# Kernel tuning notes

Measured on AMD Instinct MI355X. Metric: run time of the kernel, lower is better.

The kernel has to match this reference:

```python
import jax, jax.numpy as jnp
import numpy as np

DIM_V = 512
NUM_HEADS = 8
LN_EPS = 1e-5


def _layernorm(x):
    # LayerNorm over last dim, no affine (simplified_layer_norm=True)
    mu = jnp.mean(x, axis=-1, keepdims=True)
    var = jnp.mean(jnp.square(x - mu), axis=-1, keepdims=True)
    return (x - mu) * jax.lax.rsqrt(var + LN_EPS)


def setup_inputs() -> dict:
    key = jax.random.key(0)
    ks = jax.random.split(key, 12)
    B, Nq, Nk, dQ, dK, dV = 16, 1024, 1024, 512, 512, DIM_V
    s = 0.02
    return {
        "Q": jax.random.normal(ks[0], (B, Nq, dQ), jnp.float32),
        "K": jax.random.normal(ks[1], (B, Nk, dK), jnp.float32),
        "Wq": jax.random.normal(ks[2], (dQ, dV), jnp.float32) * s,
        "bq": jnp.zeros((dV,), jnp.float32),
        "Wk": jax.random.normal(ks[3], (dK, dV), jnp.float32) * s,
        "bk": jnp.zeros((dV,), jnp.float32),
        "Wv": jax.random.normal(ks[4], (dK, dV), jnp.float32) * s,
        "bv": jnp.zeros((dV,), jnp.float32),
        "Wo": jax.random.normal(ks[5], (dV, dV), jnp.float32) * s,
        "bo": jnp.zeros((dV,), jnp.float32),
    }


def reference(Q, K, Wq, bq, Wk, bk, Wv, bv, Wo, bo):
    H = NUM_HEADS
    dh = DIM_V // H
    q = Q @ Wq + bq            # [B, Nq, dV]
    k = K @ Wk + bk            # [B, Nk, dV]
    v = K @ Wv + bv            # [B, Nk, dV]
    B, Nq, _ = q.shape
    Nk = k.shape[1]
    qh = q.reshape(B, Nq, H, dh)
    kh = k.reshape(B, Nk, H, dh)
    vh = v.reshape(B, Nk, H, dh)
    # NOTE: faithful to source — scale by sqrt(dim_V), not sqrt(head_dim)
    scores = jnp.einsum('bqhd,bkhd->bhqk', qh, kh) / jnp.sqrt(jnp.asarray(DIM_V, q.dtype))
    A = jax.nn.softmax(scores, axis=-1)                    # [B, H, Nq, Nk]
    attn = jnp.einsum('bhqk,bkhd->bqhd', A, vh).reshape(B, Nq, DIM_V)
    O = q + attn               # residual with projected Q
    O = _layernorm(O)          # ln0 (no affine)
    O = O + jax.nn.gelu(O @ Wo + bo, approximate=False)
    O = _layernorm(O)          # ln1 (no affine)
    return O
```

## Files before the change

### kernel.cpp

```cpp
#include <hip/hip_runtime.h>
#include <hip/hip_bf16.h>
#include <math.h>

typedef __bf16 bf16;
typedef __bf16 bf16x8 __attribute__((ext_vector_type(8)));
typedef float  f32x4  __attribute__((ext_vector_type(4)));

#define MFMA16(a,b,c) __builtin_amdgcn_mfma_f32_16x16x32_bf16((a),(b),(c),0,0,0)
#define ATT_SCALE 0.0441941738241592f

__device__ __forceinline__ void async16p(const void* g, void* l) {
    __builtin_amdgcn_global_load_lds((const __attribute__((address_space(1))) void*)g,
                                     (__attribute__((address_space(3))) void*)l,
                                     16, 0, 0);
}

__global__ __launch_bounds__(256) void prep_w_kernel(
    const float* __restrict__ Wq, const float* __restrict__ Wk,
    const float* __restrict__ Wv, const float* __restrict__ Wo,
    bf16* __restrict__ WqT, bf16* __restrict__ WkT,
    bf16* __restrict__ WvT, bf16* __restrict__ WoT)
{
    __shared__ float tile[32][33];
    const int bx = blockIdx.x;
    const float* W; bf16* T;
    switch (bx >> 8) {
      case 0: W=Wq; T=WqT; break;
      case 1: W=Wk; T=WkT; break;
      case 2: W=Wv; T=WvT; break;
      default: W=Wo; T=WoT; break;
    }
    const int rest = bx & 255;
    const int k0 = (rest & 15) * 32, n0 = (rest >> 4) * 32;
    const int tx = threadIdx.x & 31, ty = threadIdx.x >> 5;
    #pragma unroll
    for (int i=0;i<32;i+=8)
        tile[ty+i][tx] = W[(size_t)(k0+ty+i)*512 + n0+tx];
    __syncthreads();
    #pragma unroll
    for (int i=0;i<32;i+=8)
        T[(size_t)(n0+ty+i)*512 + k0+tx] = (bf16)tile[tx][ty+i];
}

__global__ __launch_bounds__(256, 2) void gemm_qkv_kernel(
    const float* __restrict__ Qf, const float* __restrict__ Kf,
    const bf16* __restrict__ WqT, const bf16* __restrict__ WkT,
    const bf16* __restrict__ WvT,
    const float* __restrict__ bq, const float* __restrict__ bk,
    const float* __restrict__ bv,
    bf16* __restrict__ qbb, bf16* __restrict__ kbb, bf16* __restrict__ vT)
{
    __shared__ float As32[128*32];
    __shared__ bf16  Bs0[128*32];
    __shared__ bf16  Bs1[128*32];
    __shared__ bf16  Lt[64][136];
    const bool kv = (blockIdx.z != 0);
    const float* A   = kv ? Kf : Qf;
    const bf16*  BT0 = kv ? WkT : WqT;
    const float* b0  = kv ? bk : bq;
    bf16* C0 = kv ? kbb : qbb;

    const int m0 = blockIdx.x * 128, n0 = blockIdx.y * 128;
    const int tid = threadIdx.x;
    const int lane = tid & 63, wave = tid >> 6;
    const int qd = lane >> 4, lr = lane & 15;
    const int wm = (wave & 1) * 64, wn = (wave >> 1) * 64;

    const float* gA = A + (size_t)(m0 + (tid>>3))*512 + (((tid&7)^((tid>>3)&7))*4);
    float* lA = As32 + wave*256;
    const int bgr = ((tid&3)^((tid>>2)&3))*8;
    const bf16* gB0 = BT0 + (size_t)(n0 + (tid>>2))*512 + bgr;
    const bf16* gB1 = WvT + (size_t)(n0 + (tid>>2))*512 + bgr;
    bf16* lB0 = Bs0 + wave*512;
    bf16* lB1 = Bs1 + wave*512;

    f32x4 acc0[4][4], acc1[4][4];
    #pragma unroll
    for (int i=0;i<4;i++)
      #pragma unroll
      for (int j=0;j<4;j++) { acc0[i][j] = (f32x4){0,0,0,0}; acc1[i][j] = (f32x4){0,0,0,0}; }

    for (int k0 = 0; k0 < 512; k0 += 32) {
        __syncthreads();
        #pragma unroll
        for (int i=0;i<4;i++)
            async16p(gA + k0 + (size_t)i*32*512, lA + i*1024);
        async16p(gB0 + k0,            lB0);
        async16p(gB0 + k0 + 64*512,   lB0 + 2048);
        if (kv) {
            async16p(gB1 + k0,          lB1);
            async16p(gB1 + k0 + 64*512, lB1 + 2048);
        }
        __syncthreads();
        bf16x8 af[4], bf0[4], bf1[4];
        #pragma unroll
        for (int mi=0;mi<4;mi++) {
            int row = wm + mi*16 + lr;
            f32x4 f0 = *(f32x4*)(As32 + row*32 + (((qd*2  )^(lr&7))*4));
            f32x4 f1 = *(f32x4*)(As32 + row*32 + (((qd*2+1)^(lr&7))*4));
            bf16x8 a;
            a[0]=(bf16)f0[0]; a[1]=(bf16)f0[1]; a[2]=(bf16)f0[2]; a[3]=(bf16)f0[3];
            a[4]=(bf16)f1[0]; a[5]=(bf16)f1[1]; a[6]=(bf16)f1[2]; a[7]=(bf16)f1[3];
            af[mi] = a;
        }
        #pragma unroll
        for (int ni=0;ni<4;ni++) {
            int row = wn + ni*16 + lr;
            bf0[ni] = *(bf16x8*)(Bs0 + row*32 + ((qd^(lr&3))*8));
            if (kv) bf1[ni] = *(bf16x8*)(Bs1 + row*32 + ((qd^(lr&3))*8));
        }
        #pragma unroll
        for (int mi=0;mi<4;mi++)
          #pragma unroll
          for (int ni=0;ni<4;ni++) {
            acc0[mi][ni] = MFMA16(af[mi], bf0[ni], acc0[mi][ni]);
            if (kv) acc1[mi][ni] = MFMA16(af[mi], bf1[ni], acc1[mi][ni]);
          }
    }

    #pragma unroll
    for (int ni=0;ni<4;ni++) {
        int n = n0 + wn + ni*16 + lr;
        float bv0 = b0[n];
        #pragma unroll
        for (int mi=0;mi<4;mi++) {
            int mb = m0 + wm + mi*16 + qd*4;
            #pragma unroll
            for (int r=0;r<4;r++)
                C0[(size_t)(mb+r)*512 + n] = (bf16)(acc0[mi][ni][r] + bv0);
        }
    }
    if (kv) {
        const int b = m0 >> 10, tok0 = m0 & 1023;
        const int row = tid >> 2, ch = tid & 3;
        #pragma unroll
        for (int half = 0; half < 2; ++half) {
            __syncthreads();
            if ((wn >> 6) == half) {
                #pragma unroll
                for (int ni=0;ni<4;ni++) {
                    int nl = ni*16 + lr;
                    float bvv = bv[n0 + half*64 + nl];
                    #pragma unroll
                    for (int mi=0;mi<4;mi++)
                      #pragma unroll
                      for (int r=0;r<4;r++)
                        Lt[nl][wm + mi*16 + qd*4 + r] = (bf16)(acc1[mi][ni][r] + bvv);
                }
            }
            __syncthreads();
            const int h = (n0 >> 6) + half;
            bf16* dst = vT + ((size_t)((b*8 + h)*64 + row))*1024 + tok0 + ch*32;
            uint4 x0 = *(uint4*)(&Lt[row][ch*32]);
            uint4 x1 = *(uint4*)(&Lt[row][ch*32 + 8]);
            uint4 x2 = *(uint4*)(&Lt[row][ch*32 + 16]);
            uint4 x3 = *(uint4*)(&Lt[row][ch*32 + 24]);
            *(uint4*)(dst)      = x0;
            *(uint4*)(dst + 8)  = x1;
            *(uint4*)(dst + 16) = x2;
            *(uint4*)(dst + 24) = x3;
        }
    }
}

__global__ __launch_bounds__(256, 4) void attn_kernel(
    const bf16* __restrict__ qb, const bf16* __restrict__ kb,
    const bf16* __restrict__ vT, bf16* __restrict__ attnb)
{
    const int qt = blockIdx.x, h = blockIdx.y, b = blockIdx.z;
    const int tid = threadIdx.x, lane = tid & 63, wave = tid >> 6;
    const int qd = lane >> 4, lr = lane & 15;
    const int q0 = qt*64 + wave*16;

    __shared__ bf16 Ks[64*64];
    __shared__ bf16 Vs[64*64];
    __shared__ bf16 Pl[4][16][72];

    bf16x8 aq0, aq1;
    {
        const bf16* qrow = qb + ((size_t)(b*1024 + q0 + lr))*512 + h*64;
        aq0 = *(const bf16x8*)(qrow + qd*8);
        aq1 = *(const bf16x8*)(qrow + 32 + qd*8);
    }

    const int srow = (tid >> 3) & 7;
    const int sgr  = ((tid&7) ^ srow) * 8;
    const bf16* kgp = kb + ((size_t)(b*1024 + wave*8 + srow))*512 + h*64 + sgr;
    const bf16* vgp = vT + ((size_t)((b*8 + h)*64 + wave*8 + srow))*1024 + sgr;
    bf16* lK = Ks + wave*512;
    bf16* lV = Vs + wave*512;

    f32x4 acc[4];
    #pragma unroll
    for (int i=0;i<4;i++) acc[i] = (f32x4){0,0,0,0};
    float l[4] = {0.f,0.f,0.f,0.f};

    for (int t=0; t<16; ++t) {
        const int kk0 = t*64;
        __syncthreads();
        async16p(kgp + (size_t)kk0*512,            lK);
        async16p(kgp + (size_t)(kk0+32)*512,       lK + 2048);
        async16p(vgp + kk0,                        lV);
        async16p(vgp + (size_t)32*1024 + kk0,      lV + 2048);
        __syncthreads();

        f32x4 s[4];
        #pragma unroll
        for (int ni=0;ni<4;ni++) s[ni] = (f32x4){0,0,0,0};
        #pragma unroll
        for (int ni=0;ni<4;ni++) {
            int row = ni*16 + lr;
            bf16x8 b0 = *(bf16x8*)(Ks + row*64 + (((qd  )^(lr&7))*8));
            bf16x8 b1 = *(bf16x8*)(Ks + row*64 + (((qd+4)^(lr&7))*8));
            s[ni] = MFMA16(aq0, b0, s[ni]);
            s[ni] = MFMA16(aq1, b1, s[ni]);
        }
        #pragma unroll
        for (int ni=0;ni<4;ni++)
          #pragma unroll
          for (int r=0;r<4;r++) {
            float pv = __expf(s[ni][r] * ATT_SCALE);
            s[ni][r] = pv;
            l[r] += pv;
          }
        #pragma unroll
        for (int ni=0;ni<4;ni++)
          #pragma unroll
          for (int r=0;r<4;r++)
            Pl[wave][qd*4+r][ni*16+lr] = (bf16)s[ni][r];
        bf16x8 ap0 = *(bf16x8*)(&Pl[wave][lr][qd*8]);
        bf16x8 ap1 = *(bf16x8*)(&Pl[wave][lr][32+qd*8]);
        #pragma unroll
        for (int ni=0;ni<4;ni++) {
            int row = ni*16 + lr;
            bf16x8 v0 = *(bf16x8*)(Vs + row*64 + (((qd  )^(lr&7))*8));
            bf16x8 v1 = *(bf16x8*)(Vs + row*64 + (((qd+4)^(lr&7))*8));
            acc[ni] = MFMA16(ap0, v0, acc[ni]);
            acc[ni] = MFMA16(ap1, v1, acc[ni]);
        }
    }

    #pragma unroll
    for (int off=1; off<16; off<<=1)
      #pragma unroll
      for (int r=0;r<4;r++) l[r] += __shfl_xor(l[r], off);

    float inv[4];
    #pragma unroll
    for (int r=0;r<4;r++) inv[r] = 1.f / l[r];
    #pragma unroll
    for (int ni=0;ni<4;ni++)
      #pragma unroll
      for (int r=0;r<4;r++)
        Pl[wave][qd*4+r][ni*16+lr] = (bf16)(acc[ni][r] * inv[r]);
    bf16x8 oA = *(bf16x8*)(&Pl[wave][lr][qd*8]);
    bf16x8 oB = *(bf16x8*)(&Pl[wave][lr][32+qd*8]);
    bf16* dst = attnb + ((size_t)(b*1024 + q0 + lr))*512 + h*64;
    *(bf16x8*)(dst + qd*8)      = oA;
    *(bf16x8*)(dst + 32 + qd*8) = oB;
}

__global__ __launch_bounds__(256) void ln0_kernel(
    const bf16* __restrict__ qbb, const bf16* __restrict__ attnb,
    bf16* __restrict__ Obf, float* __restrict__ O32)
{
    const int wave = threadIdx.x >> 6, lane = threadIdx.x & 63;
    const int row = blockIdx.x*4 + wave;
    const size_t base = (size_t)row*512 + lane*8;
    bf16x8 qv = *(const bf16x8*)(qbb + base);
    bf16x8 av = *(const bf16x8*)(attnb + base);
    float x[8];
    #pragma unroll
    for (int i=0;i<8;i++) x[i] = (float)qv[i] + (float)av[i];
    float s1 = 0.f, s2 = 0.f;
    #pragma unroll
    for (int i=0;i<8;i++){ s1 += x[i]; s2 += x[i]*x[i]; }
    #pragma unroll
    for (int off=1; off<64; off<<=1) { s1 += __shfl_xor(s1, off); s2 += __shfl_xor(s2, off); }
    float mu  = s1 * (1.f/512.f);
    float var = s2 * (1.f/512.f) - mu*mu;
    float rstd = rsqrtf(var + 1e-5f);
    bf16x8 ob; float4 o0, o1;
    float y[8];
    #pragma unroll
    for (int i=0;i<8;i++) { y[i] = (x[i]-mu)*rstd; ob[i] = (bf16)y[i]; }
    o0 = (float4){y[0],y[1],y[2],y[3]};
    o1 = (float4){y[4],y[5],y[6],y[7]};
    *(bf16x8*)(Obf + base) = ob;
    *(float4*)(O32 + base)     = o0;
    *(float4*)(O32 + base + 4) = o1;
}

__global__ __launch_bounds__(256, 3) void gemm_o_kernel(
    const bf16* __restrict__ Obf, const bf16* __restrict__ WoT,
    const float* __restrict__ bo, const float* __restrict__ O32,
    float* __restrict__ x32)
{
    __shared__ bf16 As[128*32];
    __shared__ bf16 Bs[128*32];
    const int m0 = blockIdx.x * 128, n0 = blockIdx.y * 128;
    const int tid = threadIdx.x;
    const int lane = tid & 63, wave = tid >> 6;
    const int qd = lane >> 4, lr = lane & 15;
    const int wm = (wave & 1) * 64, wn = (wave >> 1) * 64;

    const int gr = ((tid&3)^((tid>>2)&3))*8;
    const bf16* gA = Obf + (size_t)(m0 + (tid>>2))*512 + gr;
    const bf16* gB = WoT + (size_t)(n0 + (tid>>2))*512 + gr;
    bf16* lA = As + wave*512;
    bf16* lB = Bs + wave*512;

    f32x4 acc[4][4];
    #pragma unroll
    for (int i=0;i<4;i++)
      #pragma unroll
      for (int j=0;j<4;j++) acc[i][j] = (f32x4){0,0,0,0};

    for (int k0 = 0; k0 < 512; k0 += 32) {
        __syncthreads();
        async16p(gA + k0,          lA);
        async16p(gA + k0 + 64*512, lA + 2048);
        async16p(gB + k0,          lB);
        async16p(gB + k0 + 64*512, lB + 2048);
        __syncthreads();
        bf16x8 af[4], bfr[4];
        #pragma unroll
        for (int mi=0;mi<4;mi++) af[mi]  = *(bf16x8*)(As + (wm+mi*16+lr)*32 + ((qd^(lr&3))*8));
        #pragma unroll
        for (int ni=0;ni<4;ni++) bfr[ni] = *(bf16x8*)(Bs + (wn+ni*16+lr)*32 + ((qd^(lr&3))*8));
        #pragma unroll
        for (int mi=0;mi<4;mi++)
          #pragma unroll
          for (int ni=0;ni<4;ni++)
            acc[mi][ni] = MFMA16(af[mi], bfr[ni], acc[mi][ni]);
    }

    #pragma unroll
    for (int ni=0;ni<4;ni++) {
        int n = n0 + wn + ni*16 + lr;
        float bv = bo[n];
        #pragma unroll
        for (int mi=0;mi<4;mi++) {
            int mb = m0 + wm + mi*16 + qd*4;
            #pragma unroll
            for (int r=0;r<4;r++) {
                float g = acc[mi][ni][r] + bv;
                float gelu = 0.5f * g * (1.f + erff(g * 0.70710678118654752f));
                size_t idx = (size_t)(mb+r)*512 + n;
                x32[idx] = O32[idx] + gelu;
            }
        }
    }
}

__global__ __launch_bounds__(256) void ln1_kernel(
    const float* __restrict__ x32, float* __restrict__ out)
{
    const int wave = threadIdx.x >> 6, lane = threadIdx.x & 63;
    const int row = blockIdx.x*4 + wave;
    const size_t base = (size_t)row*512 + lane*8;
    float4 a0 = *(const float4*)(x32 + base);
    float4 a1 = *(const float4*)(x32 + base + 4);
    float x[8] = {a0.x,a0.y,a0.z,a0.w,a1.x,a1.y,a1.z,a1.w};
    float s1 = 0.f, s2 = 0.f;
    #pragma unroll
    for (int i=0;i<8;i++){ s1 += x[i]; s2 += x[i]*x[i]; }
    #pragma unroll
    for (int off=1; off<64; off<<=1) { s1 += __shfl_xor(s1, off); s2 += __shfl_xor(s2, off); }
    float mu  = s1 * (1.f/512.f);
    float var = s2 * (1.f/512.f) - mu*mu;
    float rstd = rsqrtf(var + 1e-5f);
    float4 o0 = {(x[0]-mu)*rstd,(x[1]-mu)*rstd,(x[2]-mu)*rstd,(x[3]-mu)*rstd};
    float4 o1 = {(x[4]-mu)*rstd,(x[5]-mu)*rstd,(x[6]-mu)*rstd,(x[7]-mu)*rstd};
    *(float4*)(out + base)     = o0;
    *(float4*)(out + base + 4) = o1;
}

extern "C" void kernel_launch(void* const* d_in, const int* in_sizes, int n_in,
                              void* d_out, int out_size, void* d_ws, size_t ws_size,
                              hipStream_t stream)
{
    (void)in_sizes; (void)n_in; (void)out_size; (void)ws_size;
    const float* Q  = (const float*)d_in[0];
    const float* K  = (const float*)d_in[1];
    const float* Wq = (const float*)d_in[2];
    const float* bq = (const float*)d_in[3];
    const float* Wk = (const float*)d_in[4];
    const float* bk = (const float*)d_in[5];
    const float* Wv = (const float*)d_in[6];
    const float* bv = (const float*)d_in[7];
    const float* Wo = (const float*)d_in[8];
    const float* bo = (const float*)d_in[9];
    float* out = (float*)d_out;

    const size_t nTok = (size_t)16*1024*512;
    char* p = (char*)d_ws;
    auto alloc = [&](size_t bytes)->char* {
        char* r = p; p += (bytes + 255) & ~(size_t)255; return r;
    };
    bf16* WqT   = (bf16*)alloc(512*512*2);
    bf16* WkT   = (bf16*)alloc(512*512*2);
    bf16* WvT   = (bf16*)alloc(512*512*2);
    bf16* WoT   = (bf16*)alloc(512*512*2);
    bf16* qbb   = (bf16*)alloc(nTok*2);
    bf16* kbb   = (bf16*)alloc(nTok*2);
    bf16* vT    = (bf16*)alloc(nTok*2);
    bf16* attnb = (bf16*)alloc(nTok*2);
    bf16* Obf   = (bf16*)alloc(nTok*2);
    float* O32  = (float*)alloc(nTok*4);
    float* x32  = (float*)alloc(nTok*4);

    prep_w_kernel<<<1024, 256, 0, stream>>>(Wq, Wk, Wv, Wo, WqT, WkT, WvT, WoT);
    gemm_qkv_kernel<<<dim3(128,4,2), 256, 0, stream>>>(Q, K, WqT, WkT, WvT,
                                                       bq, bk, bv, qbb, kbb, vT);
    attn_kernel<<<dim3(16,8,16), 256, 0, stream>>>(qbb, kbb, vT, attnb);
    ln0_kernel<<<4096, 256, 0, stream>>>(qbb, attnb, Obf, O32);
    gemm_o_kernel<<<dim3(128,4), 256, 0, stream>>>(Obf, WoT, bo, O32, x32);
    ln1_kernel<<<4096, 256, 0, stream>>>(x32, out);
}
```

Measured before the change: 286.4 us.

## Split QKV GEMM by z, double-buffer attention K/V, drop fp32 intermediates

Splits the fused K/V projection GEMM into separate z-slices (Q, K, V) so each block does one output with a smaller register and LDS footprint, allowing higher occupancy. The V transpose staging buffer becomes XOR-swizzled and aliases the A tile. The attention kernel double-buffers K/V tiles, prefetching the next tile while computing the current one, and drops one barrier. The fp32 O32 and x32 intermediates are replaced by bf16 (the residual read from Obf), which cuts HBM traffic at the cost of lower precision in the residual and the final LayerNorm input.

```diff
diff --git a/kernel.cpp b/kernel.cpp
--- a/kernel.cpp
+++ b/kernel.cpp
@@ -42,7 +42,7 @@
         T[(size_t)(n0+ty+i)*512 + k0+tx] = (bf16)tile[tx][ty+i];
 }
 
-__global__ __launch_bounds__(256, 2) void gemm_qkv_kernel(
+__global__ __launch_bounds__(256, 3) void gemm_qkv_kernel(
     const float* __restrict__ Qf, const float* __restrict__ Kf,
     const bf16* __restrict__ WqT, const bf16* __restrict__ WkT,
     const bf16* __restrict__ WvT,
@@ -50,15 +50,15 @@
     const float* __restrict__ bv,
     bf16* __restrict__ qbb, bf16* __restrict__ kbb, bf16* __restrict__ vT)
 {
-    __shared__ float As32[128*32];
-    __shared__ bf16  Bs0[128*32];
-    __shared__ bf16  Bs1[128*32];
-    __shared__ bf16  Lt[64][136];
-    const bool kv = (blockIdx.z != 0);
-    const float* A   = kv ? Kf : Qf;
-    const bf16*  BT0 = kv ? WkT : WqT;
-    const float* b0  = kv ? bk : bq;
-    bf16* C0 = kv ? kbb : qbb;
+    __shared__ __align__(16) char smem[32768];
+    float* As32 = (float*)smem;
+    bf16*  Bs   = (bf16*)(smem + 16384);
+    bf16*  Lt   = (bf16*)smem;
+
+    const int z = blockIdx.z;
+    const float* A  = (z == 0) ? Qf : Kf;
+    const bf16*  BT = (z == 0) ? WqT : (z == 1) ? WkT : WvT;
+    const float* bb = (z == 0) ? bq  : (z == 1) ? bk  : bv;
 
     const int m0 = blockIdx.x * 128, n0 = blockIdx.y * 128;
     const int tid = threadIdx.x;
@@ -68,31 +68,24 @@
 
     const float* gA = A + (size_t)(m0 + (tid>>3))*512 + (((tid&7)^((tid>>3)&7))*4);
     float* lA = As32 + wave*256;
-    const int bgr = ((tid&3)^((tid>>2)&3))*8;
-    const bf16* gB0 = BT0 + (size_t)(n0 + (tid>>2))*512 + bgr;
-    const bf16* gB1 = WvT + (size_t)(n0 + (tid>>2))*512 + bgr;
-    bf16* lB0 = Bs0 + wave*512;
-    bf16* lB1 = Bs1 + wave*512;
-
-    f32x4 acc0[4][4], acc1[4][4];
+    const bf16* gB = BT + (size_t)(n0 + (tid>>2))*512 + (((tid&3)^((tid>>2)&3))*8);
+    bf16* lB = Bs + wave*512;
+
+    f32x4 acc[4][4];
     #pragma unroll
     for (int i=0;i<4;i++)
       #pragma unroll
-      for (int j=0;j<4;j++) { acc0[i][j] = (f32x4){0,0,0,0}; acc1[i][j] = (f32x4){0,0,0,0}; }
+      for (int j=0;j<4;j++) acc[i][j] = (f32x4){0,0,0,0};
 
     for (int k0 = 0; k0 < 512; k0 += 32) {
         __syncthreads();
         #pragma unroll
         for (int i=0;i<4;i++)
             async16p(gA + k0 + (size_t)i*32*512, lA + i*1024);
-        async16p(gB0 + k0,            lB0);
-        async16p(gB0 + k0 + 64*512,   lB0 + 2048);
-        if (kv) {
-            async16p(gB1 + k0,          lB1);
-            async16p(gB1 + k0 + 64*512, lB1 + 2048);
-        }
+        async16p(gB + k0,          lB);
+        async16p(gB + k0 + 64*512, lB + 2048);
         __syncthreads();
-        bf16x8 af[4], bf0[4], bf1[4];
+        bf16x8 af[4], bfr[4];
         #pragma unroll
         for (int mi=0;mi<4;mi++) {
             int row = wm + mi*16 + lr;
@@ -104,33 +97,30 @@
             af[mi] = a;
         }
         #pragma unroll
-        for (int ni=0;ni<4;ni++) {
-            int row = wn + ni*16 + lr;
-            bf0[ni] = *(bf16x8*)(Bs0 + row*32 + ((qd^(lr&3))*8));
-            if (kv) bf1[ni] = *(bf16x8*)(Bs1 + row*32 + ((qd^(lr&3))*8));
-        }
+        for (int ni=0;ni<4;ni++)
+            bfr[ni] = *(bf16x8*)(Bs + (wn+ni*16+lr)*32 + ((qd^(lr&3))*8));
         #pragma unroll
         for (int mi=0;mi<4;mi++)
           #pragma unroll
-          for (int ni=0;ni<4;ni++) {
-            acc0[mi][ni] = MFMA16(af[mi], bf0[ni], acc0[mi][ni]);
-            if (kv) acc1[mi][ni] = MFMA16(af[mi], bf1[ni], acc1[mi][ni]);
-          }
-    }
-
-    #pragma unroll
-    for (int ni=0;ni<4;ni++) {
-        int n = n0 + wn + ni*16 + lr;
-        float bv0 = b0[n];
-        #pragma unroll
-        for (int mi=0;mi<4;mi++) {
-            int mb = m0 + wm + mi*16 + qd*4;
+          for (int ni=0;ni<4;ni++)
+            acc[mi][ni] = MFMA16(af[mi], bfr[ni], acc[mi][ni]);
+    }
+
+    if (z < 2) {
+        bf16* C = (z == 0) ? qbb : kbb;
+        #pragma unroll
+        for (int ni=0;ni<4;ni++) {
+            int n = n0 + wn + ni*16 + lr;
+            float bv0 = bb[n];
             #pragma unroll
-            for (int r=0;r<4;r++)
-                C0[(size_t)(mb+r)*512 + n] = (bf16)(acc0[mi][ni][r] + bv0);
-        }
-    }
-    if (kv) {
+            for (int mi=0;mi<4;mi++) {
+                int mb = m0 + wm + mi*16 + qd*4;
+                #pragma unroll
+                for (int r=0;r<4;r++)
+                    C[(size_t)(mb+r)*512 + n] = (bf16)(acc[mi][ni][r] + bv0);
+            }
+        }
+    } else {
         const int b = m0 >> 10, tok0 = m0 & 1023;
         const int row = tid >> 2, ch = tid & 3;
         #pragma unroll
@@ -140,30 +130,30 @@
                 #pragma unroll
                 for (int ni=0;ni<4;ni++) {
                     int nl = ni*16 + lr;
-                    float bvv = bv[n0 + half*64 + nl];
+                    float bvv = bb[n0 + half*64 + nl];
                     #pragma unroll
                     for (int mi=0;mi<4;mi++)
                       #pragma unroll
-                      for (int r=0;r<4;r++)
-                        Lt[nl][wm + mi*16 + qd*4 + r] = (bf16)(acc1[mi][ni][r] + bvv);
+                      for (int r=0;r<4;r++) {
+                        int col = wm + mi*16 + qd*4 + r;
+                        Lt[nl*128 + ((((col>>3)^(nl&7))<<3) | (col&7))]
+                            = (bf16)(acc[mi][ni][r] + bvv);
+                      }
                 }
             }
             __syncthreads();
             const int h = (n0 >> 6) + half;
             bf16* dst = vT + ((size_t)((b*8 + h)*64 + row))*1024 + tok0 + ch*32;
-            uint4 x0 = *(uint4*)(&Lt[row][ch*32]);
-            uint4 x1 = *(uint4*)(&Lt[row][ch*32 + 8]);
-            uint4 x2 = *(uint4*)(&Lt[row][ch*32 + 16]);
-            uint4 x3 = *(uint4*)(&Lt[row][ch*32 + 24]);
-            *(uint4*)(dst)      = x0;
-            *(uint4*)(dst + 8)  = x1;
-            *(uint4*)(dst + 16) = x2;
-            *(uint4*)(dst + 24) = x3;
-        }
-    }
-}
-
-__global__ __launch_bounds__(256, 4) void attn_kernel(
+            #pragma unroll
+            for (int s=0;s<4;s++) {
+                int g = (ch*4 + s) ^ (row & 7);
+                *(uint4*)(dst + s*8) = *(uint4*)(Lt + row*128 + g*8);
+            }
+        }
+    }
+}
+
+__global__ __launch_bounds__(256, 3) void attn_kernel(
     const bf16* __restrict__ qb, const bf16* __restrict__ kb,
     const bf16* __restrict__ vT, bf16* __restrict__ attnb)
 {
@@ -172,8 +162,8 @@
     const int qd = lane >> 4, lr = lane & 15;
     const int q0 = qt*64 + wave*16;
 
-    __shared__ bf16 Ks[64*64];
-    __shared__ bf16 Vs[64*64];
+    __shared__ bf16 Ks[2][64*64];
+    __shared__ bf16 Vs[2][64*64];
     __shared__ bf16 Pl[4][16][72];
 
     bf16x8 aq0, aq1;
@@ -187,8 +177,12 @@
     const int sgr  = ((tid&7) ^ srow) * 8;
     const bf16* kgp = kb + ((size_t)(b*1024 + wave*8 + srow))*512 + h*64 + sgr;
     const bf16* vgp = vT + ((size_t)((b*8 + h)*64 + wave*8 + srow))*1024 + sgr;
-    bf16* lK = Ks + wave*512;
-    bf16* lV = Vs + wave*512;
+    const int woff = wave*512;
+
+    async16p(kgp,                    &Ks[0][woff]);
+    async16p(kgp + (size_t)32*512,   &Ks[0][woff + 2048]);
+    async16p(vgp,                    &Vs[0][woff]);
+    async16p(vgp + (size_t)32*1024,  &Vs[0][woff + 2048]);
 
     f32x4 acc[4];
     #pragma unroll
@@ -196,13 +190,18 @@
     float l[4] = {0.f,0.f,0.f,0.f};
 
     for (int t=0; t<16; ++t) {
-        const int kk0 = t*64;
+        const int cur = t & 1;
         __syncthreads();
-        async16p(kgp + (size_t)kk0*512,            lK);
-        async16p(kgp + (size_t)(kk0+32)*512,       lK + 2048);
-        async16p(vgp + kk0,                        lV);
-        async16p(vgp + (size_t)32*1024 + kk0,      lV + 2048);
-        __syncthreads();
+        if (t < 15) {
+            const int nb = 1 - cur;
+            const size_t kk = (size_t)(t+1)*64;
+            async16p(kgp + kk*512,             &Ks[nb][woff]);
+            async16p(kgp + (kk+32)*512,        &Ks[nb][woff + 2048]);
+            async16p(vgp + kk,                 &Vs[nb][woff]);
+            async16p(vgp + (size_t)32*1024+kk, &Vs[nb][woff + 2048]);
+        }
+        const bf16* kc = &Ks[cur][0];
+        const bf16* vc = &Vs[cur][0];
 
         f32x4 s[4];
         #pragma unroll
@@ -210,8 +209,8 @@
         #pragma unroll
         for (int ni=0;ni<4;ni++) {
             int row = ni*16 + lr;
-            bf16x8 b0 = *(bf16x8*)(Ks + row*64 + (((qd  )^(lr&7))*8));
-            bf16x8 b1 = *(bf16x8*)(Ks + row*64 + (((qd+4)^(lr&7))*8));
+            bf16x8 b0 = *(bf16x8*)(kc + row*64 + (((qd  )^(lr&7))*8));
+            bf16x8 b1 = *(bf16x8*)(kc + row*64 + (((qd+4)^(lr&7))*8));
             s[ni] = MFMA16(aq0, b0, s[ni]);
             s[ni] = MFMA16(aq1, b1, s[ni]);
         }
@@ -233,8 +232,8 @@
         #pragma unroll
         for (int ni=0;ni<4;ni++) {
             int row = ni*16 + lr;
-            bf16x8 v0 = *(bf16x8*)(Vs + row*64 + (((qd  )^(lr&7))*8));
-            bf16x8 v1 = *(bf16x8*)(Vs + row*64 + (((qd+4)^(lr&7))*8));
+            bf16x8 v0 = *(bf16x8*)(vc + row*64 + (((qd  )^(lr&7))*8));
+            bf16x8 v1 = *(bf16x8*)(vc + row*64 + (((qd+4)^(lr&7))*8));
             acc[ni] = MFMA16(ap0, v0, acc[ni]);
             acc[ni] = MFMA16(ap1, v1, acc[ni]);
         }
@@ -262,7 +261,7 @@
 
 __global__ __launch_bounds__(256) void ln0_kernel(
     const bf16* __restrict__ qbb, const bf16* __restrict__ attnb,
-    bf16* __restrict__ Obf, float* __restrict__ O32)
+    bf16* __restrict__ Obf)
 {
     const int wave = threadIdx.x >> 6, lane = threadIdx.x & 63;
     const int row = blockIdx.x*4 + wave;
@@ -280,21 +279,15 @@
     float mu  = s1 * (1.f/512.f);
     float var = s2 * (1.f/512.f) - mu*mu;
     float rstd = rsqrtf(var + 1e-5f);
-    bf16x8 ob; float4 o0, o1;
-    float y[8];
-    #pragma unroll
-    for (int i=0;i<8;i++) { y[i] = (x[i]-mu)*rstd; ob[i] = (bf16)y[i]; }
-    o0 = (float4){y[0],y[1],y[2],y[3]};
-    o1 = (float4){y[4],y[5],y[6],y[7]};
+    bf16x8 ob;
+    #pragma unroll
+    for (int i=0;i<8;i++) ob[i] = (bf16)((x[i]-mu)*rstd);
     *(bf16x8*)(Obf + base) = ob;
-    *(float4*)(O32 + base)     = o0;
-    *(float4*)(O32 + base + 4) = o1;
 }
 
 __global__ __launch_bounds__(256, 3) void gemm_o_kernel(
     const bf16* __restrict__ Obf, const bf16* __restrict__ WoT,
-    const float* __restrict__ bo, const float* __restrict__ O32,
-    float* __restrict__ x32)
+    const float* __restrict__ bo, bf16* __restrict__ xb)
 {
     __shared__ bf16 As[128*32];
     __shared__ bf16 Bs[128*32];
@@ -347,21 +340,22 @@
                 float g = acc[mi][ni][r] + bv;
                 float gelu = 0.5f * g * (1.f + erff(g * 0.70710678118654752f));
                 size_t idx = (size_t)(mb+r)*512 + n;
-                x32[idx] = O32[idx] + gelu;
+                xb[idx] = (bf16)((float)Obf[idx] + gelu);
             }
         }
     }
 }
 
 __global__ __launch_bounds__(256) void ln1_kernel(
-    const float* __restrict__ x32, float* __restrict__ out)
+    const bf16* __restrict__ xb, float* __restrict__ out)
 {
     const int wave = threadIdx.x >> 6, lane = threadIdx.x & 63;
     const int row = blockIdx.x*4 + wave;
     const size_t base = (size_t)row*512 + lane*8;
-    float4 a0 = *(const float4*)(x32 + base);
-    float4 a1 = *(const float4*)(x32 + base + 4);
-    float x[8] = {a0.x,a0.y,a0.z,a0.w,a1.x,a1.y,a1.z,a1.w};
+    bf16x8 xv = *(const bf16x8*)(xb + base);
+    float x[8];
+    #pragma unroll
+    for (int i=0;i<8;i++) x[i] = (float)xv[i];
     float s1 = 0.f, s2 = 0.f;
     #pragma unroll
     for (int i=0;i<8;i++){ s1 += x[i]; s2 += x[i]*x[i]; }
@@ -407,14 +401,13 @@
     bf16* vT    = (bf16*)alloc(nTok*2);
     bf16* attnb = (bf16*)alloc(nTok*2);
     bf16* Obf   = (bf16*)alloc(nTok*2);
-    float* O32  = (float*)alloc(nTok*4);
-    float* x32  = (float*)alloc(nTok*4);
+    bf16* xb    = (bf16*)alloc(nTok*2);
 
     prep_w_kernel<<<1024, 256, 0, stream>>>(Wq, Wk, Wv, Wo, WqT, WkT, WvT, WoT);
-    gemm_qkv_kernel<<<dim3(128,4,2), 256, 0, stream>>>(Q, K, WqT, WkT, WvT,
+    gemm_qkv_kernel<<<dim3(128,4,3), 256, 0, stream>>>(Q, K, WqT, WkT, WvT,
                                                        bq, bk, bv, qbb, kbb, vT);
     attn_kernel<<<dim3(16,8,16), 256, 0, stream>>>(qbb, kbb, vT, attnb);
-    ln0_kernel<<<4096, 256, 0, stream>>>(qbb, attnb, Obf, O32);
-    gemm_o_kernel<<<dim3(128,4), 256, 0, stream>>>(Obf, WoT, bo, O32, x32);
-    ln1_kernel<<<4096, 256, 0, stream>>>(x32, out);
-}
+    ln0_kernel<<<4096, 256, 0, stream>>>(qbb, attnb, Obf);
+    gemm_o_kernel<<<dim3(128,4), 256, 0, stream>>>(Obf, WoT, bo, xb);
+    ln1_kernel<<<4096, 256, 0, stream>>>(xb, out);
+}
```

Measured after the change: 283.8 us. Within noise of the previous version (-0.9%).
